# Kernel tuning notes

Hardware: AMD Instinct MI355X
Metric: run time of the kernel (lower is better)

## Reference

```python
import jax, jax.numpy as jnp
import numpy as np

N = 2048

def setup_inputs() -> dict:
    key = jax.random.key(0)
    k0, k1, k2, k3 = jax.random.split(key, 4)
    return {
        "input": jax.random.normal(k0, (N, N), dtype=jnp.float32),
        "weight1": jax.random.normal(k1, (N, N), dtype=jnp.float32),
        "weight2": jax.random.normal(k2, (N, N), dtype=jnp.float32),
        "weight3": jax.random.normal(k3, (N, N), dtype=jnp.float32),
    }

def reference(input, weight1, weight2, weight3):
    # Faithful translation of the torch DAG (duplicate mm kept: t4 == t2,
    # so t8 is mathematically zero, but we preserve the original math).
    t1 = input @ weight1
    t2 = input @ weight2
    t3 = weight3 @ weight3
    t4 = input @ weight2
    t5 = t1 * weight1
    t6 = (t5 @ input) * weight1
    t7 = t1 * t2 + t1 + t3
    t8 = t2 - t4
    t9 = t7 * t8 + t6 * t3
    t11 = t3 * t9
    t12 = t3 * (t1 @ input) * t6
    t13 = t7 + t11
    t14 = t8 + t12
    t15 = t13 + t14
    return t15
```

## Files before the change

kernel.cpp:

```cpp
#include <hip/hip_runtime.h>
#include <hip/hip_bf16.h>
#include <stdint.h>

#define NN 2048
#define BM 128
#define BN 64
#define BK 32

typedef __bf16 bf16;
typedef __bf16 bf16x8 __attribute__((ext_vector_type(8)));
typedef __bf16 bf16x4 __attribute__((ext_vector_type(4)));
typedef float f32x4 __attribute__((ext_vector_type(4)));

__device__ __forceinline__ void async_copy16(bf16* lds, const bf16* g) {
    __builtin_amdgcn_global_load_lds(
        (const __attribute__((address_space(1))) unsigned int*)g,
        (__attribute__((address_space(3))) unsigned int*)lds,
        16, 0, 0);
}

struct CastArgs {
    const float* in[4];
    bf16*        outT[4];
    bf16*        outN[4];
};

__global__ void transpose_cast_kernel(CastArgs args) {
    const float* __restrict__ in = args.in[blockIdx.z];
    bf16* __restrict__ outT      = args.outT[blockIdx.z];
    bf16* __restrict__ outN      = args.outN[blockIdx.z];
    __shared__ float tile[32][33];
    const int bx = blockIdx.x * 32, by = blockIdx.y * 32;
    const int tx = threadIdx.x, ty = threadIdx.y;
#pragma unroll
    for (int i = 0; i < 32; i += 8) {
        float v = in[(size_t)(by + ty + i) * NN + bx + tx];
        tile[ty + i][tx] = v;
        if (outN) outN[(size_t)(by + ty + i) * NN + bx + tx] = (bf16)v;
    }
    __syncthreads();
#pragma unroll
    for (int i = 0; i < 32; i += 8)
        outT[(size_t)(bx + ty + i) * NN + by + tx] = (bf16)tile[tx][ty + i];
}

struct GemmArgs {
    const bf16* A[3];
    const bf16* Bt[3];
    float*      C[3];
};

__global__ __launch_bounds__(256) void gemm_bt_batched(GemmArgs args) {
    const bf16* __restrict__ A  = args.A[blockIdx.z];
    const bf16* __restrict__ Bt = args.Bt[blockIdx.z];
    float* __restrict__ C       = args.C[blockIdx.z];

    __shared__ bf16 As[BM * BK];
    __shared__ bf16 Bs[BN * BK];

    const int t  = threadIdx.x;
    const int bm = blockIdx.x * BM;
    const int bn = blockIdx.y * BN;

    const int row0 = t >> 2;
    const int qp   = t & 3;
    const int col0 = ((qp ^ ((row0 >> 1) & 3)) << 3);
    const int off0 = t * 8;

    const bf16* gA0 = A  + (size_t)(bm + row0) * NN + col0;
    const bf16* gB0 = Bt + (size_t)(bn + row0) * NN + col0;

    const int wave = t >> 6;
    const int lane = t & 63;
    const int wm   = (wave >> 1) * 64;
    const int wn   = (wave & 1) * 32;
    const int lrow = lane & 15;
    const int q    = lane >> 4;
    const int qe   = (q ^ ((lrow >> 1) & 3)) << 3;

    f32x4 acc[4][2];
#pragma unroll
    for (int i = 0; i < 4; ++i)
#pragma unroll
        for (int j = 0; j < 2; ++j) acc[i][j] = (f32x4){0.f, 0.f, 0.f, 0.f};

    for (int k0 = 0; k0 < NN; k0 += BK) {
        async_copy16(&As[off0],           gA0 + k0);
        async_copy16(&As[off0 + 64 * BK], gA0 + (size_t)64 * NN + k0);
        async_copy16(&Bs[off0],           gB0 + k0);
        __syncthreads();

        bf16x8 af[4], bfr[2];
#pragma unroll
        for (int i = 0; i < 4; ++i)
            af[i] = *(const bf16x8*)&As[(wm + i * 16 + lrow) * BK + qe];
#pragma unroll
        for (int j = 0; j < 2; ++j)
            bfr[j] = *(const bf16x8*)&Bs[(wn + j * 16 + lrow) * BK + qe];

#pragma unroll
        for (int i = 0; i < 4; ++i)
#pragma unroll
            for (int j = 0; j < 2; ++j)
                acc[i][j] = __builtin_amdgcn_mfma_f32_16x16x32_bf16(
                    af[i], bfr[j], acc[i][j], 0, 0, 0);
        __syncthreads();
    }

#pragma unroll
    for (int i = 0; i < 4; ++i)
#pragma unroll
        for (int j = 0; j < 2; ++j)
#pragma unroll
            for (int r = 0; r < 4; ++r)
                C[(size_t)(bm + wm + i * 16 + q * 4 + r) * NN +
                  (bn + wn + j * 16 + lrow)] = acc[i][j][r];
}

__global__ void post_m1_kernel(const float* __restrict__ M1,
                               const float* __restrict__ W1,
                               bf16* __restrict__ M1bf,
                               bf16* __restrict__ B1bf) {
    const size_t i = ((size_t)blockIdx.x * 256 + threadIdx.x) * 4;
    const float4 m = *(const float4*)&M1[i];
    const float4 w = *(const float4*)&W1[i];
    bf16x4 mb = {(bf16)m.x, (bf16)m.y, (bf16)m.z, (bf16)m.w};
    bf16x4 bb = {(bf16)(m.x * w.x), (bf16)(m.y * w.y),
                 (bf16)(m.z * w.z), (bf16)(m.w * w.w)};
    *(bf16x4*)&M1bf[i] = mb;
    *(bf16x4*)&B1bf[i] = bb;
}

__global__ void epilogue_kernel(const float* __restrict__ M1,
                                const float* __restrict__ M3,
                                const float* __restrict__ M4,
                                const float* __restrict__ M5,
                                const float* __restrict__ W1,
                                float* __restrict__ out) {
    const size_t i = ((size_t)blockIdx.x * 256 + threadIdx.x) * 4;
    const float4 m1 = *(const float4*)&M1[i];
    const float4 m3 = *(const float4*)&M3[i];
    const float4 m4 = *(const float4*)&M4[i];
    const float4 m5 = *(const float4*)&M5[i];
    const float4 w1 = *(const float4*)&W1[i];
    const float4 m2 = *(const float4*)&out[i];
    float4 r;
    r.x = m1.x * m2.x + m1.x + m3.x + m3.x * (m4.x * w1.x) * (m3.x + m5.x);
    r.y = m1.y * m2.y + m1.y + m3.y + m3.y * (m4.y * w1.y) * (m3.y + m5.y);
    r.z = m1.z * m2.z + m1.z + m3.z + m3.z * (m4.z * w1.z) * (m3.z + m5.z);
    r.w = m1.w * m2.w + m1.w + m3.w + m3.w * (m4.w * w1.w) * (m3.w + m5.w);
    *(float4*)&out[i] = r;
}

extern "C" void kernel_launch(void* const* d_in, const int* in_sizes, int n_in,
                              void* d_out, int out_size, void* d_ws, size_t ws_size,
                              hipStream_t stream) {
    const float* A  = (const float*)d_in[0];
    const float* W1 = (const float*)d_in[1];
    const float* W2 = (const float*)d_in[2];
    const float* W3 = (const float*)d_in[3];
    float* out = (float*)d_out;

    const size_t P = (size_t)NN * NN;
    char* ws = (char*)d_ws;

    bf16* Abf  = (bf16*)ws;
    bf16* At   = Abf + P;
    bf16* W1t  = At + P;
    bf16* W2t  = W1t + P;
    bf16* W3bf = W2t + P;
    bf16* W3t  = W3bf + P;
    float* M1  = (float*)(W3t + P);
    float* M3  = M1 + P;
    float* M4  = M3 + P;
    float* M5  = M4 + P;

    CastArgs ca;
    ca.in[0] = A;  ca.outT[0] = At;  ca.outN[0] = Abf;
    ca.in[1] = W1; ca.outT[1] = W1t; ca.outN[1] = nullptr;
    ca.in[2] = W2; ca.outT[2] = W2t; ca.outN[2] = nullptr;
    ca.in[3] = W3; ca.outT[3] = W3t; ca.outN[3] = W3bf;
    transpose_cast_kernel<<<dim3(NN / 32, NN / 32, 4), dim3(32, 8), 0, stream>>>(ca);

    GemmArgs g3;
    g3.A[0] = Abf;  g3.Bt[0] = W1t; g3.C[0] = M1;
    g3.A[1] = Abf;  g3.Bt[1] = W2t; g3.C[1] = out;
    g3.A[2] = W3bf; g3.Bt[2] = W3t; g3.C[2] = M3;
    gemm_bt_batched<<<dim3(NN / BM, NN / BN, 3), 256, 0, stream>>>(g3);

    bf16* M1bf = W2t;
    bf16* B1bf = W3bf;
    post_m1_kernel<<<(P / 4) / 256, 256, 0, stream>>>(M1, W1, M1bf, B1bf);

    GemmArgs g2;
    g2.A[0] = M1bf; g2.Bt[0] = At; g2.C[0] = M5;
    g2.A[1] = B1bf; g2.Bt[1] = At; g2.C[1] = M4;
    g2.A[2] = M1bf; g2.Bt[2] = At; g2.C[2] = M5;
    gemm_bt_batched<<<dim3(NN / BM, NN / BN, 2), 256, 0, stream>>>(g2);

    epilogue_kernel<<<(P / 4) / 256, 256, 0, stream>>>(M1, M3, M4, M5, W1, out);
}
```

Before: 273.4 us.

## Triple-buffer GEMM async loads, widen tile to 128x128, vectorize transpose-cast

The GEMM moves from a single LDS buffer with two barriers per k-step to a three-stage ring of LDS buffers. Loads for two tiles ahead are issued and waited on with explicit vmcnt counts, so global-to-LDS traffic overlaps the MFMA work. BN grows to 128, giving each wave a 64x64 tile (4x4 MFMA accumulators) for more reuse and fewer blocks, at the cost of more registers and LDS. The transpose-cast kernel now uses 64x64 tiles with float4 loads and bf16x8 transposed stores to cut memory transactions.

```diff
diff --git a/kernel.cpp b/kernel.cpp
--- a/kernel.cpp
+++ b/kernel.cpp
@@ -4,7 +4,7 @@
 
 #define NN 2048
 #define BM 128
-#define BN 64
+#define BN 128
 #define BK 32
 
 typedef __bf16 bf16;
@@ -19,29 +19,52 @@
         16, 0, 0);
 }
 
+#define WAIT_VM8() asm volatile("s_waitcnt vmcnt(8)" ::: "memory")
+#define WAIT_VM4() asm volatile("s_waitcnt vmcnt(4)" ::: "memory")
+#define WAIT_VM0() asm volatile("s_waitcnt vmcnt(0)" ::: "memory")
+#define BAR()                                  \
+    do {                                       \
+        asm volatile("" ::: "memory");         \
+        __builtin_amdgcn_s_barrier();          \
+        asm volatile("" ::: "memory");         \
+    } while (0)
+
 struct CastArgs {
     const float* in[4];
     bf16*        outT[4];
     bf16*        outN[4];
 };
 
-__global__ void transpose_cast_kernel(CastArgs args) {
+__global__ __launch_bounds__(256) void transpose_cast_kernel(CastArgs args) {
     const float* __restrict__ in = args.in[blockIdx.z];
     bf16* __restrict__ outT      = args.outT[blockIdx.z];
     bf16* __restrict__ outN      = args.outN[blockIdx.z];
-    __shared__ float tile[32][33];
-    const int bx = blockIdx.x * 32, by = blockIdx.y * 32;
-    const int tx = threadIdx.x, ty = threadIdx.y;
-#pragma unroll
-    for (int i = 0; i < 32; i += 8) {
-        float v = in[(size_t)(by + ty + i) * NN + bx + tx];
-        tile[ty + i][tx] = v;
-        if (outN) outN[(size_t)(by + ty + i) * NN + bx + tx] = (bf16)v;
+    __shared__ float tile[64][65];
+    const int bx = blockIdx.x * 64;
+    const int by = blockIdx.y * 64;
+    const int t  = threadIdx.x;
+    const int tc = t & 15, tr = t >> 4;
+#pragma unroll
+    for (int p = 0; p < 4; ++p) {
+        const int r = tr + p * 16;
+        const float4 v = *(const float4*)&in[(size_t)(by + r) * NN + bx + tc * 4];
+        tile[r][tc * 4 + 0] = v.x; tile[r][tc * 4 + 1] = v.y;
+        tile[r][tc * 4 + 2] = v.z; tile[r][tc * 4 + 3] = v.w;
+        if (outN) {
+            bf16x4 b = {(bf16)v.x, (bf16)v.y, (bf16)v.z, (bf16)v.w};
+            *(bf16x4*)&outN[(size_t)(by + r) * NN + bx + tc * 4] = b;
+        }
     }
     __syncthreads();
-#pragma unroll
-    for (int i = 0; i < 32; i += 8)
-        outT[(size_t)(bx + ty + i) * NN + by + tx] = (bf16)tile[tx][ty + i];
+    const int cc = t >> 2, e = t & 3;
+#pragma unroll
+    for (int u = 0; u < 2; ++u) {
+        const int r0 = e * 16 + u * 8;
+        bf16x8 b;
+#pragma unroll
+        for (int i = 0; i < 8; ++i) b[i] = (bf16)tile[r0 + i][cc];
+        *(bf16x8*)&outT[(size_t)(bx + cc) * NN + by + r0] = b;
+    }
 }
 
 struct GemmArgs {
@@ -55,8 +78,8 @@
     const bf16* __restrict__ Bt = args.Bt[blockIdx.z];
     float* __restrict__ C       = args.C[blockIdx.z];
 
-    __shared__ bf16 As[BM * BK];
-    __shared__ bf16 Bs[BN * BK];
+    __shared__ bf16 As0[BM * BK], As1[BM * BK], As2[BM * BK];
+    __shared__ bf16 Bs0[BN * BK], Bs1[BN * BK], Bs2[BN * BK];
 
     const int t  = threadIdx.x;
     const int bm = blockIdx.x * BM;
@@ -73,44 +96,58 @@
     const int wave = t >> 6;
     const int lane = t & 63;
     const int wm   = (wave >> 1) * 64;
-    const int wn   = (wave & 1) * 32;
+    const int wn   = (wave & 1) * 64;
     const int lrow = lane & 15;
     const int q    = lane >> 4;
     const int qe   = (q ^ ((lrow >> 1) & 3)) << 3;
 
-    f32x4 acc[4][2];
+    f32x4 acc[4][4];
 #pragma unroll
     for (int i = 0; i < 4; ++i)
 #pragma unroll
-        for (int j = 0; j < 2; ++j) acc[i][j] = (f32x4){0.f, 0.f, 0.f, 0.f};
-
-    for (int k0 = 0; k0 < NN; k0 += BK) {
-        async_copy16(&As[off0],           gA0 + k0);
-        async_copy16(&As[off0 + 64 * BK], gA0 + (size_t)64 * NN + k0);
-        async_copy16(&Bs[off0],           gB0 + k0);
-        __syncthreads();
-
-        bf16x8 af[4], bfr[2];
+        for (int j = 0; j < 4; ++j) acc[i][j] = (f32x4){0.f, 0.f, 0.f, 0.f};
+
+    auto issue = [&](bf16* As, bf16* Bs, int kt) {
+        const int kof = kt * BK;
+        async_copy16(&As[off0],           gA0 + kof);
+        async_copy16(&As[off0 + 64 * BK], gA0 + (size_t)64 * NN + kof);
+        async_copy16(&Bs[off0],           gB0 + kof);
+        async_copy16(&Bs[off0 + 64 * BK], gB0 + (size_t)64 * NN + kof);
+    };
+    auto compute = [&](const bf16* As, const bf16* Bs) {
+        bf16x8 af[4], bfr[4];
 #pragma unroll
         for (int i = 0; i < 4; ++i)
             af[i] = *(const bf16x8*)&As[(wm + i * 16 + lrow) * BK + qe];
 #pragma unroll
-        for (int j = 0; j < 2; ++j)
+        for (int j = 0; j < 4; ++j)
             bfr[j] = *(const bf16x8*)&Bs[(wn + j * 16 + lrow) * BK + qe];
-
 #pragma unroll
         for (int i = 0; i < 4; ++i)
 #pragma unroll
-            for (int j = 0; j < 2; ++j)
+            for (int j = 0; j < 4; ++j)
                 acc[i][j] = __builtin_amdgcn_mfma_f32_16x16x32_bf16(
                     af[i], bfr[j], acc[i][j], 0, 0, 0);
-        __syncthreads();
+    };
+
+    issue(As0, Bs0, 0);
+    issue(As1, Bs1, 1);
+
+#pragma unroll 1
+    for (int kt = 0; kt < 60; kt += 3) {
+        issue(As2, Bs2, kt + 2); WAIT_VM8(); BAR(); compute(As0, Bs0); BAR();
+        issue(As0, Bs0, kt + 3); WAIT_VM8(); BAR(); compute(As1, Bs1); BAR();
+        issue(As1, Bs1, kt + 4); WAIT_VM8(); BAR(); compute(As2, Bs2); BAR();
     }
+    issue(As2, Bs2, 62); WAIT_VM8(); BAR(); compute(As0, Bs0); BAR();
+    issue(As0, Bs0, 63); WAIT_VM8(); BAR(); compute(As1, Bs1); BAR();
+    WAIT_VM4(); BAR(); compute(As2, Bs2); BAR();
+    WAIT_VM0(); BAR(); compute(As0, Bs0);
 
 #pragma unroll
     for (int i = 0; i < 4; ++i)
 #pragma unroll
-        for (int j = 0; j < 2; ++j)
+        for (int j = 0; j < 4; ++j)
 #pragma unroll
             for (int r = 0; r < 4; ++r)
                 C[(size_t)(bm + wm + i * 16 + q * 4 + r) * NN +
@@ -180,7 +217,7 @@
     ca.in[1] = W1; ca.outT[1] = W1t; ca.outN[1] = nullptr;
     ca.in[2] = W2; ca.outT[2] = W2t; ca.outN[2] = nullptr;
     ca.in[3] = W3; ca.outT[3] = W3t; ca.outN[3] = W3bf;
-    transpose_cast_kernel<<<dim3(NN / 32, NN / 32, 4), dim3(32, 8), 0, stream>>>(ca);
+    transpose_cast_kernel<<<dim3(NN / 64, NN / 64, 4), 256, 0, stream>>>(ca);
 
     GemmArgs g3;
     g3.A[0] = Abf;  g3.Bt[0] = W1t; g3.C[0] = M1;
```

After: 237.6 us. -13.1%, faster.
